# Performance work log

Measured on AMD Instinct MI355X. Metric: run time of the kernel, lower is better.

## Reference

```python
import jax, jax.numpy as jnp
import numpy as np

N_NODES = 50000
IN_DIM = 512
OUT_DIM = 128
N_EDGES = 1600000


def setup_inputs() -> dict:
    key = jax.random.key(0)
    k1, k2, k3, k4, k5 = jax.random.split(key, 5)
    x = jax.random.normal(k1, (N_NODES, IN_DIM), dtype=jnp.float32)
    weight = jax.random.normal(k2, (IN_DIM, OUT_DIM), dtype=jnp.float32)
    edge_row = jax.random.randint(k3, (N_EDGES,), 0, N_NODES, dtype=jnp.int32)
    edge_col = jax.random.randint(k4, (N_EDGES,), 0, N_NODES, dtype=jnp.int32)
    edge_val = jax.random.uniform(k5, (N_EDGES,), dtype=jnp.float32)
    return {"x": x, "weight": weight, "edge_row": edge_row,
            "edge_col": edge_col, "edge_val": edge_val}


def reference(x, weight, edge_row, edge_col, edge_val):
    # Dense feature transform: xw = x @ W   [N, OUT_DIM]
    xw = jnp.matmul(x, weight)
    # Sparse adjacency SpMM in COO form: out[r] += val * xw[c]
    msgs = edge_val[:, None] * xw[edge_col]          # [E, OUT_DIM]
    out = jax.ops.segment_sum(msgs, edge_row, num_segments=N_NODES)
    # activation=True, bias=False per init defaults
    return jax.nn.relu(out)
```

## Files before the change

### kernel.cpp

```cpp
#include <hip/hip_runtime.h>

#define N_NODES 50000
#define IN_DIM 512
#define OUT_DIM 128
#define N_EDGES 1600000

#define NPART 8
#define ROWS_PER_PART 6250
#define CAP 96

#define G_GEMM 782
#define G_BUILD 754

typedef __attribute__((ext_vector_type(8))) short short8;
typedef __attribute__((ext_vector_type(4))) float floatx4;

__device__ __forceinline__ ushort f2bf(float f) {
    uint u = __float_as_uint(f);
    u += 0x7FFFu + ((u >> 16) & 1u);
    return (ushort)(u >> 16);
}

constexpr size_t OFF_XWB   = 0;
constexpr size_t OFF_WT    = 12800000;
constexpr size_t OFF_CUR_F = 12931072;
constexpr size_t OFF_SRT_F = 13131264;
constexpr size_t OFF_OFFS  = 12931072;
constexpr size_t OFF_CUR_S = 13131264;
constexpr size_t OFF_SRT_S = 13331456;

__global__ __launch_bounds__(256) void conv_wt(const float* __restrict__ w,
                                               ushort* __restrict__ wt) {
    int t = blockIdx.x * 256 + threadIdx.x;
    if (t < IN_DIM * OUT_DIM) {
        int k = t >> 7;
        int c = t & 127;
        wt[(size_t)c * IN_DIM + k] = f2bf(w[t]);
    }
}

__device__ __forceinline__ void gemm_tile_body(const float* __restrict__ x,
                                               const ushort* __restrict__ wt,
                                               ushort* __restrict__ xwb,
                                               int block_row, char* Alds, char* Blds,
                                               int tid) {
    const int w = tid >> 6;
    const int lane = tid & 63;

    floatx4 acc[8];
#pragma unroll
    for (int i = 0; i < 8; ++i) acc[i] = (floatx4){0.f, 0.f, 0.f, 0.f};

    for (int k0 = 0; k0 < IN_DIM; k0 += 64) {
#pragma unroll
        for (int it = 0; it < 4; ++it) {
            int f4 = tid + it * 256;
            int r = f4 >> 4;
            int f4c = f4 & 15;
            int grow = block_row + r;
            float4 v = make_float4(0.f, 0.f, 0.f, 0.f);
            if (grow < N_NODES)
                v = *reinterpret_cast<const float4*>(&x[(size_t)grow * IN_DIM + k0 + f4c * 4]);
            ushort4 b = make_ushort4(f2bf(v.x), f2bf(v.y), f2bf(v.z), f2bf(v.w));
            int off = r * 128 + ((f4c * 8) ^ ((r & 7) << 4));
            *reinterpret_cast<ushort4*>(Alds + off) = b;
        }
#pragma unroll
        for (int it = 0; it < 4; ++it) {
            int j = tid * 16 + it * 4096;
            int c = j >> 7;
            int inner = j & 127;
            ulonglong2 v = *reinterpret_cast<const ulonglong2*>(
                reinterpret_cast<const char*>(wt) + (size_t)c * 1024 + k0 * 2 + inner);
            int off = c * 128 + (inner ^ ((c & 7) << 4));
            *reinterpret_cast<ulonglong2*>(Blds + off) = v;
        }
        __syncthreads();

#pragma unroll
        for (int kb = 0; kb < 2; ++kb) {
            int ar = w * 16 + (lane & 15);
            int koffb = kb * 64 + (lane >> 4) * 16;
            short8 afrag = *reinterpret_cast<const short8*>(
                Alds + ar * 128 + (koffb ^ ((ar & 7) << 4)));
#pragma unroll
            for (int ct = 0; ct < 8; ++ct) {
                int bc = ct * 16 + (lane & 15);
                short8 bfrag = *reinterpret_cast<const short8*>(
                    Blds + bc * 128 + (koffb ^ ((bc & 7) << 4)));
                acc[ct] = __builtin_amdgcn_mfma_f32_16x16x32_bf16(afrag, bfrag, acc[ct], 0, 0, 0);
            }
        }
        __syncthreads();
    }

    const int orow0 = block_row + w * 16 + (lane >> 4) * 4;
    const int ocol = lane & 15;
#pragma unroll
    for (int ct = 0; ct < 8; ++ct) {
#pragma unroll
        for (int i = 0; i < 4; ++i) {
            int grow = orow0 + i;
            if (grow < N_NODES)
                xwb[(size_t)grow * OUT_DIM + ct * 16 + ocol] = f2bf(acc[ct][i]);
        }
    }
}

__device__ __forceinline__ void build_body4(const int* __restrict__ erow,
                                            const int* __restrict__ ecol,
                                            const float* __restrict__ eval_,
                                            int* __restrict__ cur,
                                            uint* __restrict__ srt,
                                            int part, int k, int np, int tid) {
    const int lo = part * ROWS_PER_PART;
    const int hi = lo + ROWS_PER_PART;
    const int stride = np * 256;
    for (int e = k * 256 + tid; e < N_EDGES; e += stride) {
        int r = __builtin_nontemporal_load(&erow[e]);
        if (r >= lo && r < hi) {
            int n = atomicAdd(&cur[r], 1);
            if (n < CAP) {
                int c = __builtin_nontemporal_load(&ecol[e]);
                float v = __builtin_nontemporal_load(&eval_[e]);
                srt[(size_t)r * CAP + n] = ((uint)f2bf(v) << 16) | (uint)c;
            }
        }
    }
}

__global__ __launch_bounds__(256) void fat_gemm_build(const float* __restrict__ x,
                                                      const ushort* __restrict__ wt,
                                                      ushort* __restrict__ xwb,
                                                      const int* __restrict__ erow,
                                                      const int* __restrict__ ecol,
                                                      const float* __restrict__ eval_,
                                                      int* __restrict__ cur,
                                                      uint* __restrict__ srt) {
    __shared__ char lds[24576];
    const int tid = threadIdx.x;
    if (blockIdx.x < G_GEMM) {
        gemm_tile_body(x, wt, xwb, blockIdx.x * 64, lds, lds + 8192, tid);
    } else {
        int j = blockIdx.x - G_GEMM;
        int p = blockIdx.x & (NPART - 1);
        int k = j >> 3;
        int np = (p >= 6) ? 95 : 94;
        build_body4(erow, ecol, eval_, cur, srt, p, k, np, tid);
    }
}

__global__ __launch_bounds__(256) void gemm_xw_mfma(const float* __restrict__ x,
                                                    const ushort* __restrict__ wt,
                                                    ushort* __restrict__ xwb) {
    __shared__ char lds[24576];
    gemm_tile_body(x, wt, xwb, blockIdx.x * 64, lds, lds + 8192, threadIdx.x);
}

__global__ __launch_bounds__(256) void aggregate_cap4(const uint* __restrict__ srt,
                                                      const int* __restrict__ cur,
                                                      const ushort* __restrict__ xwb,
                                                      float* __restrict__ out) {
    int row = blockIdx.x * 4 + (threadIdx.x >> 6);
    if (row >= N_NODES) return;
    int lane = threadIdx.x & 63;
    int cnt = cur[row];
    if (cnt > CAP) cnt = CAP;
    const uint* seg = srt + (size_t)row * CAP;
    const uint* base = reinterpret_cast<const uint*>(xwb);

    float a0 = 0.f, a1 = 0.f, b0 = 0.f, b1 = 0.f;
    float c0 = 0.f, c1 = 0.f, d0 = 0.f, d1 = 0.f;
    int i = 0;
    for (; i + 3 < cnt; i += 4) {
        uint4 p4 = *reinterpret_cast<const uint4*>(&seg[i]);
        uint m0 = base[(size_t)(p4.x & 0xFFFFu) * 64 + lane];
        uint m1 = base[(size_t)(p4.y & 0xFFFFu) * 64 + lane];
        uint m2 = base[(size_t)(p4.z & 0xFFFFu) * 64 + lane];
        uint m3 = base[(size_t)(p4.w & 0xFFFFu) * 64 + lane];
        float v0 = __uint_as_float(p4.x & 0xFFFF0000u);
        float v1 = __uint_as_float(p4.y & 0xFFFF0000u);
        float v2 = __uint_as_float(p4.z & 0xFFFF0000u);
        float v3 = __uint_as_float(p4.w & 0xFFFF0000u);
        a0 = fmaf(v0, __uint_as_float(m0 << 16), a0);
        a1 = fmaf(v0, __uint_as_float(m0 & 0xFFFF0000u), a1);
        b0 = fmaf(v1, __uint_as_float(m1 << 16), b0);
        b1 = fmaf(v1, __uint_as_float(m1 & 0xFFFF0000u), b1);
        c0 = fmaf(v2, __uint_as_float(m2 << 16), c0);
        c1 = fmaf(v2, __uint_as_float(m2 & 0xFFFF0000u), c1);
        d0 = fmaf(v3, __uint_as_float(m3 << 16), d0);
        d1 = fmaf(v3, __uint_as_float(m3 & 0xFFFF0000u), d1);
    }
    for (; i < cnt; ++i) {
        uint pk = seg[i];
        uint m = base[(size_t)(pk & 0xFFFFu) * 64 + lane];
        float v = __uint_as_float(pk & 0xFFFF0000u);
        a0 = fmaf(v, __uint_as_float(m << 16), a0);
        a1 = fmaf(v, __uint_as_float(m & 0xFFFF0000u), a1);
    }
    float s0 = (a0 + b0) + (c0 + d0);
    float s1 = (a1 + b1) + (c1 + d1);
    float2 r = make_float2(fmaxf(s0, 0.f), fmaxf(s1, 0.f));
    *reinterpret_cast<float2*>(&out[(size_t)row * OUT_DIM + lane * 2]) = r;
}

__global__ __launch_bounds__(256) void hist_part(const int* __restrict__ erow,
                                                 int* __restrict__ cnt) {
    const int part = blockIdx.x & (NPART - 1);
    const int sub = blockIdx.x >> 3;
    const int lo = part * ROWS_PER_PART;
    const int hi = lo + ROWS_PER_PART;
    for (int e = sub * 256 + threadIdx.x; e < N_EDGES; e += 65536) {
        int r = erow[e];
        if (r >= lo && r < hi) atomicAdd(&cnt[r], 1);
    }
}

__global__ __launch_bounds__(1024) void scan_offsets(int* __restrict__ offs) {
    __shared__ int partials[1024];
    const int tid = threadIdx.x;
    const int CHUNK = (N_NODES + 1023) / 1024;
    int begin = 1 + tid * CHUNK;
    int end = begin + CHUNK;
    if (end > N_NODES + 1) end = N_NODES + 1;

    int sum = 0;
    for (int i = begin; i < end; ++i) sum += offs[i];
    partials[tid] = sum;
    __syncthreads();
    for (int d = 1; d < 1024; d <<= 1) {
        int v = (tid >= d) ? partials[tid - d] : 0;
        __syncthreads();
        partials[tid] += v;
        __syncthreads();
    }
    int run = (tid == 0) ? 0 : partials[tid - 1];
    for (int i = begin; i < end; ++i) {
        run += offs[i];
        offs[i] = run;
    }
}

__global__ __launch_bounds__(256) void build_part(const int* __restrict__ erow,
                                                  const int* __restrict__ ecol,
                                                  const float* __restrict__ eval_,
                                                  const int* __restrict__ offs,
                                                  int* __restrict__ cur,
                                                  int2* __restrict__ srt) {
    const int part = blockIdx.x & (NPART - 1);
    const int sub = blockIdx.x >> 3;
    const int lo = part * ROWS_PER_PART;
    const int hi = lo + ROWS_PER_PART;
    for (int e = sub * 256 + threadIdx.x; e < N_EDGES; e += 65536) {
        int r = erow[e];
        if (r >= lo && r < hi) {
            int pos = offs[r] + atomicAdd(&cur[r], 1);
            srt[pos] = make_int2(ecol[e], __float_as_int(eval_[e]));
        }
    }
}

__global__ __launch_bounds__(256) void aggregate_rows(const int2* __restrict__ srt,
                                                      const int* __restrict__ offs,
                                                      const ushort* __restrict__ xwb,
                                                      float* __restrict__ out) {
    int row = blockIdx.x * 4 + (threadIdx.x >> 6);
    if (row >= N_NODES) return;
    int lane = threadIdx.x & 63;
    int start = offs[row];
    int end = offs[row + 1];
    const uint* base = reinterpret_cast<const uint*>(xwb);

    float a0 = 0.f, a1 = 0.f;
    for (int i = start; i < end; ++i) {
        int2 p = srt[i];
        uint m = base[(size_t)p.x * 64 + lane];
        float v = __int_as_float(p.y);
        a0 = fmaf(v, __uint_as_float(m << 16), a0);
        a1 = fmaf(v, __uint_as_float(m & 0xFFFF0000u), a1);
    }
    float2 r = make_float2(fmaxf(a0, 0.f), fmaxf(a1, 0.f));
    *reinterpret_cast<float2*>(&out[(size_t)row * OUT_DIM + lane * 2]) = r;
}

extern "C" void kernel_launch(void* const* d_in, const int* in_sizes, int n_in,
                              void* d_out, int out_size, void* d_ws, size_t ws_size,
                              hipStream_t stream) {
    const float* x     = (const float*)d_in[0];
    const float* w     = (const float*)d_in[1];
    const int*   erow  = (const int*)d_in[2];
    const int*   ecol  = (const int*)d_in[3];
    const float* eval_ = (const float*)d_in[4];
    float* out = (float*)d_out;

    char* ws = (char*)d_ws;
    ushort* xwb = (ushort*)(ws + OFF_XWB);
    ushort* wt  = (ushort*)(ws + OFF_WT);

    conv_wt<<<(IN_DIM * OUT_DIM + 255) / 256, 256, 0, stream>>>(w, wt);

    const size_t need_fast = OFF_SRT_F + (size_t)N_NODES * CAP * sizeof(uint);
    if (ws_size >= need_fast) {
        int*  cur = (int*)(ws + OFF_CUR_F);
        uint* srt = (uint*)(ws + OFF_SRT_F);
        hipMemsetAsync(ws + OFF_CUR_F, 0, (size_t)N_NODES * sizeof(int), stream);
        fat_gemm_build<<<G_GEMM + G_BUILD, 256, 0, stream>>>(x, wt, xwb, erow, ecol,
                                                             eval_, cur, srt);
        aggregate_cap4<<<(N_NODES + 3) / 4, 256, 0, stream>>>(srt, cur, xwb, out);
    } else {
        int*  offs = (int*)(ws + OFF_OFFS);
        int*  cur  = (int*)(ws + OFF_CUR_S);
        int2* srt  = (int2*)(ws + OFF_SRT_S);
        hipMemsetAsync(ws + OFF_OFFS, 0, OFF_SRT_S - OFF_OFFS, stream);
        hist_part<<<2048, 256, 0, stream>>>(erow, offs + 1);
        scan_offsets<<<1, 1024, 0, stream>>>(offs);
        gemm_xw_mfma<<<(N_NODES + 63) / 64, 256, 0, stream>>>(x, wt, xwb);
        build_part<<<2048, 256, 0, stream>>>(erow, ecol, eval_, offs, cur, srt);
        aggregate_rows<<<(N_NODES + 3) / 4, 256, 0, stream>>>(srt, offs, xwb, out);
    }
}
```

Before: 218.1 us.

## Split fused GEMM+build kernel into separate launches with half-range build passes

The fused kernel that ran the GEMM tiles and the COO bucket build side by side is replaced by two sequential launches: a standalone build kernel with 2048 blocks over 8 row partitions, followed by the MFMA GEMM. Each build block now makes two passes over the edge list, covering half of its partition's row range per pass, so each pass's atomics and scattered writes hit a smaller row window. The aggregate kernel also switches to nontemporal loads of the packed edge lists and nontemporal stores of the output. The cost is that GEMM and build no longer overlap, and the edge row array is read twice per partition.

Result: faster. 212.4 us (-2.6%).

```diff
diff --git a/kernel.cpp b/kernel.cpp
--- a/kernel.cpp
+++ b/kernel.cpp
@@ -7,13 +7,13 @@
 
 #define NPART 8
 #define ROWS_PER_PART 6250
+#define HALF_RANGE 3125
 #define CAP 96
-
-#define G_GEMM 782
-#define G_BUILD 754
 
 typedef __attribute__((ext_vector_type(8))) short short8;
 typedef __attribute__((ext_vector_type(4))) float floatx4;
+typedef __attribute__((ext_vector_type(2))) float floatx2;
+typedef __attribute__((ext_vector_type(4))) uint uintx4;
 
 __device__ __forceinline__ ushort f2bf(float f) {
     uint u = __float_as_uint(f);
@@ -107,54 +107,36 @@
     }
 }
 
-__device__ __forceinline__ void build_body4(const int* __restrict__ erow,
-                                            const int* __restrict__ ecol,
-                                            const float* __restrict__ eval_,
-                                            int* __restrict__ cur,
-                                            uint* __restrict__ srt,
-                                            int part, int k, int np, int tid) {
-    const int lo = part * ROWS_PER_PART;
-    const int hi = lo + ROWS_PER_PART;
-    const int stride = np * 256;
-    for (int e = k * 256 + tid; e < N_EDGES; e += stride) {
-        int r = __builtin_nontemporal_load(&erow[e]);
-        if (r >= lo && r < hi) {
-            int n = atomicAdd(&cur[r], 1);
-            if (n < CAP) {
-                int c = __builtin_nontemporal_load(&ecol[e]);
-                float v = __builtin_nontemporal_load(&eval_[e]);
-                srt[(size_t)r * CAP + n] = ((uint)f2bf(v) << 16) | (uint)c;
-            }
-        }
-    }
-}
-
-__global__ __launch_bounds__(256) void fat_gemm_build(const float* __restrict__ x,
-                                                      const ushort* __restrict__ wt,
-                                                      ushort* __restrict__ xwb,
-                                                      const int* __restrict__ erow,
-                                                      const int* __restrict__ ecol,
-                                                      const float* __restrict__ eval_,
-                                                      int* __restrict__ cur,
-                                                      uint* __restrict__ srt) {
-    __shared__ char lds[24576];
-    const int tid = threadIdx.x;
-    if (blockIdx.x < G_GEMM) {
-        gemm_tile_body(x, wt, xwb, blockIdx.x * 64, lds, lds + 8192, tid);
-    } else {
-        int j = blockIdx.x - G_GEMM;
-        int p = blockIdx.x & (NPART - 1);
-        int k = j >> 3;
-        int np = (p >= 6) ? 95 : 94;
-        build_body4(erow, ecol, eval_, cur, srt, p, k, np, tid);
-    }
-}
-
 __global__ __launch_bounds__(256) void gemm_xw_mfma(const float* __restrict__ x,
                                                     const ushort* __restrict__ wt,
                                                     ushort* __restrict__ xwb) {
     __shared__ char lds[24576];
     gemm_tile_body(x, wt, xwb, blockIdx.x * 64, lds, lds + 8192, threadIdx.x);
+}
+
+__global__ __launch_bounds__(256) void build_part4(const int* __restrict__ erow,
+                                                   const int* __restrict__ ecol,
+                                                   const float* __restrict__ eval_,
+                                                   int* __restrict__ cur,
+                                                   uint* __restrict__ srt) {
+    const int part = blockIdx.x & (NPART - 1);
+    const int sub = blockIdx.x >> 3;
+#pragma unroll
+    for (int phase = 0; phase < 2; ++phase) {
+        const int lo = part * ROWS_PER_PART + phase * HALF_RANGE;
+        const int hi = lo + HALF_RANGE;
+        for (int e = sub * 256 + threadIdx.x; e < N_EDGES; e += 65536) {
+            int r = __builtin_nontemporal_load(&erow[e]);
+            if (r >= lo && r < hi) {
+                int n = atomicAdd(&cur[r], 1);
+                if (n < CAP) {
+                    int c = __builtin_nontemporal_load(&ecol[e]);
+                    float v = __builtin_nontemporal_load(&eval_[e]);
+                    srt[(size_t)r * CAP + n] = ((uint)f2bf(v) << 16) | (uint)c;
+                }
+            }
+        }
+    }
 }
 
 __global__ __launch_bounds__(256) void aggregate_cap4(const uint* __restrict__ srt,
@@ -173,7 +155,7 @@
     float c0 = 0.f, c1 = 0.f, d0 = 0.f, d1 = 0.f;
     int i = 0;
     for (; i + 3 < cnt; i += 4) {
-        uint4 p4 = *reinterpret_cast<const uint4*>(&seg[i]);
+        uintx4 p4 = __builtin_nontemporal_load(reinterpret_cast<const uintx4*>(&seg[i]));
         uint m0 = base[(size_t)(p4.x & 0xFFFFu) * 64 + lane];
         uint m1 = base[(size_t)(p4.y & 0xFFFFu) * 64 + lane];
         uint m2 = base[(size_t)(p4.z & 0xFFFFu) * 64 + lane];
@@ -200,8 +182,8 @@
     }
     float s0 = (a0 + b0) + (c0 + d0);
     float s1 = (a1 + b1) + (c1 + d1);
-    float2 r = make_float2(fmaxf(s0, 0.f), fmaxf(s1, 0.f));
-    *reinterpret_cast<float2*>(&out[(size_t)row * OUT_DIM + lane * 2]) = r;
+    floatx2 r = {fmaxf(s0, 0.f), fmaxf(s1, 0.f)};
+    __builtin_nontemporal_store(r, reinterpret_cast<floatx2*>(&out[(size_t)row * OUT_DIM + lane * 2]));
 }
 
 __global__ __launch_bounds__(256) void hist_part(const int* __restrict__ erow,
@@ -303,15 +285,15 @@
     if (ws_size >= need_fast) {
         int*  cur = (int*)(ws + OFF_CUR_F);
         uint* srt = (uint*)(ws + OFF_SRT_F);
-        hipMemsetAsync(ws + OFF_CUR_F, 0, (size_t)N_NODES * sizeof(int), stream);
-        fat_gemm_build<<<G_GEMM + G_BUILD, 256, 0, stream>>>(x, wt, xwb, erow, ecol,
-                                                             eval_, cur, srt);
+        (void)hipMemsetAsync(ws + OFF_CUR_F, 0, (size_t)N_NODES * sizeof(int), stream);
+        build_part4<<<2048, 256, 0, stream>>>(erow, ecol, eval_, cur, srt);
+        gemm_xw_mfma<<<(N_NODES + 63) / 64, 256, 0, stream>>>(x, wt, xwb);
         aggregate_cap4<<<(N_NODES + 3) / 4, 256, 0, stream>>>(srt, cur, xwb, out);
     } else {
         int*  offs = (int*)(ws + OFF_OFFS);
         int*  cur  = (int*)(ws + OFF_CUR_S);
         int2* srt  = (int2*)(ws + OFF_SRT_S);
-        hipMemsetAsync(ws + OFF_OFFS, 0, OFF_SRT_S - OFF_OFFS, stream);
+        (void)hipMemsetAsync(ws + OFF_OFFS, 0, OFF_SRT_S - OFF_OFFS, stream);
         hist_part<<<2048, 256, 0, stream>>>(erow, offs + 1);
         scan_offsets<<<1, 1024, 0, stream>>>(offs);
         gemm_xw_mfma<<<(N_NODES + 63) / 64, 256, 0, stream>>>(x, wt, xwb);
```
